# Performance work log

Measured on AMD Instinct MI355X. Metric: run time of the kernel, lower is better.

## Reference

```python
import jax, jax.numpy as jnp
import numpy as np

B, T, C = 2, 2048, 1024
NH = 16
HS = C // NH

def setup_inputs() -> dict:
    key = jax.random.key(0)
    ks = jax.random.split(key, 5)
    x = jax.random.normal(ks[0], (B, T, C), dtype=jnp.float32)
    scale = 1.0 / np.sqrt(C)
    Wk = jax.random.normal(ks[1], (C, C), dtype=jnp.float32) * scale
    bk = jax.random.normal(ks[2], (C,), dtype=jnp.float32) * scale
    Wv = jax.random.normal(ks[3], (C, C), dtype=jnp.float32) * scale
    bv = jax.random.normal(ks[4], (C,), dtype=jnp.float32) * scale
    return {"x": x, "Wk": Wk, "bk": bk, "Wv": Wv, "bv": bv}

def reference(x, Wk, bk, Wv, bv):
    b, t, c = x.shape
    # projections: key and value are Dense; query is identity (as in source)
    k = (x @ Wk + bk).reshape(b, t, NH, HS).transpose(0, 2, 1, 3)  # b nh T hs
    q = x.reshape(b, t, NH, HS).transpose(0, 2, 1, 3)              # b nh T hs
    v = (x @ Wv + bv).reshape(b, t, NH, HS).transpose(0, 2, 1, 3)  # b nh T hs
    # NOTE: source computes logits = K @ Q^T (no 1/sqrt(d) scaling)
    logits = jnp.einsum('bhid,bhjd->bhij', k, q)                   # b nh T T
    causal = jnp.tril(jnp.ones((t, t), dtype=bool))                # True where allowed
    masked = jnp.where(causal[None, None, :, :], logits, -jnp.inf)
    att = jax.nn.softmax(masked, axis=-1)
    y = jnp.einsum('bhij,bhjd->bhid', att, v)                      # b nh T hs
    return y.transpose(0, 2, 1, 3).reshape(b, t, c)
```

## Files before the change

### kernel.cpp

```cpp
#include <hip/hip_runtime.h>
#include <cstdint>
#include <cstddef>

#define BB  2
#define TT  2048
#define CC  1024
#define NHH 16
#define HSS 64
#define BT  (BB*TT)

typedef unsigned short u16;
typedef unsigned int u32;
typedef _Float16 f16;
typedef __attribute__((ext_vector_type(8))) _Float16 f16x8;
typedef __attribute__((ext_vector_type(8))) __bf16 bf16x8;
typedef __attribute__((ext_vector_type(4))) float f32x4;

__device__ __forceinline__ u16 f2bf(float f) {
    union { float f; u32 u; } x; x.f = f;
    return (u16)((x.u + 0x7fffu + ((x.u >> 16) & 1u)) >> 16);
}
__device__ __forceinline__ u16 f2h(float f) {
    union { f16 h; u16 u; } x; x.h = (f16)f;
    return x.u;
}
__device__ __forceinline__ u32 cvtpk_bf16(float lo, float hi) {
    u32 r;
    asm("v_cvt_pk_bf16_f32 %0, %1, %2" : "=v"(r) : "v"(lo), "v"(hi));
    return r;
}

#define MFMA_BF(a,b,c) __builtin_amdgcn_mfma_f32_16x16x32_bf16((a),(b),(c),0,0,0)
#define MFMA_F16(a,b,c) __builtin_amdgcn_mfma_f32_16x16x32_f16((a),(b),(c),0,0,0)

__device__ __forceinline__ void gld16(const u16* g, u16* l) {
    __builtin_amdgcn_global_load_lds(
        (const __attribute__((address_space(1))) unsigned int*)g,
        (__attribute__((address_space(3))) unsigned int*)l, 16, 0, 0);
}

__global__ __launch_bounds__(256) void convert_x(
    const float* __restrict__ X, u16* __restrict__ Xf)
{
    const int idx = (blockIdx.x * 256 + threadIdx.x) * 8;
    const float4 a = *(const float4*)&X[idx];
    const float4 b = *(const float4*)&X[idx + 4];
    float v[8] = {a.x, a.y, a.z, a.w, b.x, b.y, b.z, b.w};
    union { uint4 u; u16 s[8]; } H;
    #pragma unroll
    for (int u = 0; u < 8; ++u) H.s[u] = f2h(v[u]);
    *(uint4*)&Xf[idx] = H.u;
}

__global__ __launch_bounds__(256) void convert_w(
    const float* __restrict__ Wk, const float* __restrict__ Wv,
    u16* __restrict__ WkT, u16* __restrict__ WvT)
{
    const bool isK = (blockIdx.z == 0);
    const float* W = isK ? Wk : Wv;
    u16* WT = isK ? WkT : WvT;
    __shared__ __align__(16) u16 LH[64][72];
    const int tid = threadIdx.x;
    const int k0 = blockIdx.y * 64, n0 = blockIdx.x * 64;
    {
        const int row = tid >> 2, coff = (tid & 3) * 16;
        const float* g = &W[(size_t)(k0 + row) * CC + n0 + coff];
        #pragma unroll
        for (int u = 0; u < 16; ++u) LH[row][coff + u] = f2h(g[u]);
    }
    __syncthreads();
    {
        const int n = tid >> 2, kc = (tid & 3) * 16;
        union { uint4 u[2]; u16 s[16]; } Hq;
        #pragma unroll
        for (int u = 0; u < 16; ++u) Hq.s[u] = LH[kc + u][n];
        uint4* ph = (uint4*)&WT[(size_t)(n0 + n) * CC + k0 + kc];
        ph[0] = Hq.u[0]; ph[1] = Hq.u[1];
    }
}

__global__ __launch_bounds__(256) void proj_kernel(
    const u16* __restrict__ Xf, const u16* __restrict__ WkT,
    const u16* __restrict__ WvT,
    const float* __restrict__ bk, const float* __restrict__ bv,
    u16* __restrict__ Kf, u16* __restrict__ Vt)
{
    __shared__ u16 SM[4][8192];

    const int id = blockIdx.x;
    const int xcd = id & 7, idx = id >> 3;
    const int z = idx >> 5, rem = idx & 31;
    const int n0 = (rem & 7) * 128;
    const int m0 = (xcd * 4 + (rem >> 3)) * 128;
    const bool isK = (z == 0);
    const u16* WT = isK ? WkT : WvT;

    const int tid = threadIdx.x;
    const int w = tid >> 6, lane = tid & 63;
    const int quad = lane >> 4, l15 = lane & 15;
    const int wm = (w >> 1) * 64, wn = (w & 1) * 64;

    const u16* src = (w < 2) ? Xf : WT;
    const int rb = (w < 2) ? m0 : n0;
    int srow[8], scg[8];
    #pragma unroll
    for (int t = 0; t < 8; ++t) {
        int ci = (w & 1) * 512 + t * 64 + lane;
        srow[t] = ci >> 3;
        scg[t] = ((ci & 7) - srow[t]) & 7;
    }
    const int sbase = (w & 1) * 4096;

    f32x4 acc[4][4] = {};

    {
        u16* dst = ((w < 2) ? SM[0] : SM[2]) + sbase;
        #pragma unroll
        for (int t = 0; t < 8; ++t)
            gld16(src + (size_t)(rb + srow[t]) * CC + scg[t] * 8, dst + t * 512);
    }

    for (int ki = 0; ki < 16; ++ki) {
        const int buf = ki & 1;
        __syncthreads();
        if (ki < 15) {
            u16* dst = ((w < 2) ? SM[buf ^ 1] : SM[2 + (buf ^ 1)]) + sbase;
            const int k0n = (ki + 1) * 64;
            #pragma unroll
            for (int t = 0; t < 8; ++t)
                gld16(src + (size_t)(rb + srow[t]) * CC + k0n + scg[t] * 8,
                      dst + t * 512);
        }
        const u16* Ab = SM[buf];
        const u16* Bb = SM[2 + buf];
        #pragma unroll
        for (int kk = 0; kk < 2; ++kk) {
            f16x8 ah[4];
            #pragma unroll
            for (int i = 0; i < 4; ++i) {
                const int row = wm + i * 16 + l15;
                const int cp = ((kk * 4 + quad + row) & 7) * 8;
                ah[i] = *(const f16x8*)&Ab[row * 64 + cp];
            }
            #pragma unroll
            for (int j = 0; j < 4; ++j) {
                const int rowb = wn + j * 16 + l15;
                const int cpb = ((kk * 4 + quad + rowb) & 7) * 8;
                f16x8 bh_ = *(const f16x8*)&Bb[rowb * 64 + cpb];
                #pragma unroll
                for (int i = 0; i < 4; ++i)
                    acc[i][j] = MFMA_F16(ah[i], bh_, acc[i][j]);
            }
        }
    }

    __syncthreads();
    u16* XL = &SM[0][0];

    if (isK) {
        #pragma unroll
        for (int j = 0; j < 4; ++j) {
            const float bias = bk[n0 + wn + j * 16 + l15];
            #pragma unroll
            for (int i = 0; i < 4; ++i)
                #pragma unroll
                for (int r = 0; r < 4; ++r)
                    XL[(wm + i * 16 + quad * 4 + r) * 136 + wn + j * 16 + l15] =
                        f2h(acc[i][j][r] + bias);
        }
        __syncthreads();
        const int r = tid >> 1, half = tid & 1;
        #pragma unroll
        for (int t = 0; t < 8; ++t)
            *(uint4*)&Kf[(size_t)(m0 + r) * CC + n0 + half * 64 + t * 8] =
                *(const uint4*)&XL[r * 136 + half * 64 + t * 8];
    } else {
        #pragma unroll
        for (int j = 0; j < 4; ++j) {
            const float bias = bv[n0 + wn + j * 16 + l15];
            #pragma unroll
            for (int i = 0; i < 4; ++i) {
                uint2 pk;
                pk.x = (u32)f2bf(acc[i][j][0] + bias) |
                       ((u32)f2bf(acc[i][j][1] + bias) << 16);
                pk.y = (u32)f2bf(acc[i][j][2] + bias) |
                       ((u32)f2bf(acc[i][j][3] + bias) << 16);
                *(uint2*)&XL[(wn + j * 16 + l15) * 136 + wm + i * 16 + quad * 4] = pk;
            }
        }
        __syncthreads();
        const int nl = tid >> 1, half = tid & 1;
        const int d = (n0 + nl) & (HSS - 1), hh = (n0 + nl) >> 6;
        const int bb = m0 >> 11, tb = (m0 & (TT - 1)) + half * 64;
        const size_t gb = ((size_t)(bb * NHH + hh) * HSS + d) * TT + tb;
        #pragma unroll
        for (int t = 0; t < 8; ++t)
            *(uint4*)&Vt[gb + t * 8] = *(const uint4*)&XL[nl * 136 + half * 64 + t * 8];
    }
}

__global__ __launch_bounds__(256) void attn_kernel(
    const u16* __restrict__ Xf, const u16* __restrict__ Kf,
    const u16* __restrict__ Vt, float* __restrict__ out)
{
    __shared__ u16 Xs[2][4096];
    __shared__ u16 Vs[2][4096];
    __shared__ __align__(16) u16 Ps[4][2][1152];

    const int L = blockIdx.x;
    const int xcd = L & 7, k = (L >> 3) & 15, grp = L >> 7;
    const int hb = xcd + 8 * grp;
    const int h = hb & (NHH - 1), b = hb >> 4;
    const int iA = k, iB = 31 - k;
    const int i0A = iA * 64, i0B = iB * 64;

    const int tid = threadIdx.x;
    const int w = tid >> 6, lane = tid & 63;
    const int quad = lane >> 4, l15 = lane & 15;
    const size_t rowbase = (size_t)b * TT;
    const int hd = h * HSS;
    const size_t vgbase = (size_t)(b * NHH + h) * HSS * TT;

    bf16x8 ones;
    { union { u32 u[4]; bf16x8 v; } o;
      #pragma unroll
      for (int i = 0; i < 4; ++i) o.u[i] = 0x3F803F80u;
      ones = o.v; }

    f16x8 qA[2], qB[2];
    #pragma unroll
    for (int c = 0; c < 2; ++c) {
        qA[c] = *(const f16x8*)&Kf[(rowbase + i0A + w * 16 + l15) * CC + hd + c * 32 + quad * 8];
        qB[c] = *(const f16x8*)&Kf[(rowbase + i0B + w * 16 + l15) * CC + hd + c * 32 + quad * 8];
    }

    int crow[2], ccg[2], cbase[2];
    #pragma unroll
    for (int t = 0; t < 2; ++t) {
        const int ci = t * 256 + tid;
        crow[t] = ci >> 3;
        ccg[t] = ((ci & 7) - crow[t]) & 7;
        cbase[t] = (t * 256 + w * 64) * 8;
    }
    const u16* gx[2]; const u16* gv[2];
    #pragma unroll
    for (int t = 0; t < 2; ++t) {
        gx[t] = Xf + (rowbase + crow[t]) * CC + hd + ccg[t] * 8;
        gv[t] = Vt + vgbase + (size_t)crow[t] * TT + ccg[t] * 8;
    }

    #pragma unroll
    for (int t = 0; t < 2; ++t) {
        gld16(gx[t], Xs[0] + cbase[t]);
        gld16(gv[t], Vs[0] + cbase[t]);
    }

    f32x4 oA[4] = {}, oB[4] = {};
    f32x4 laA = {}, laB = {};

    for (int jt = 0; jt <= iB; ++jt) {
        const int buf = jt & 1;
        __syncthreads();
        if (jt < iB) {
            const int j0n = (jt + 1) * 64;
            #pragma unroll
            for (int t = 0; t < 2; ++t) {
                gld16(gx[t] + (size_t)j0n * CC, Xs[buf ^ 1] + cbase[t]);
                gld16(gv[t] + j0n, Vs[buf ^ 1] + cbase[t]);
            }
        }
        const bool doA = (jt <= iA);

        f32x4 sB[4], sA[4];
        #pragma unroll
        for (int nt = 0; nt < 4; ++nt) {
            const int krow = nt * 16 + l15;
            f16x8 x0 = *(const f16x8*)&Xs[buf][krow * 64 + ((quad + krow) & 7) * 8];
            f16x8 x1 = *(const f16x8*)&Xs[buf][krow * 64 + ((quad + 4 + krow) & 7) * 8];
            f32x4 z = {-20.f, -20.f, -20.f, -20.f};
            z = MFMA_F16(x0, qB[0], z);
            z = MFMA_F16(x1, qB[1], z);
            sB[nt] = z;
            if (doA) {
                f32x4 y = {-20.f, -20.f, -20.f, -20.f};
                y = MFMA_F16(x0, qA[0], y);
                y = MFMA_F16(x1, qA[1], y);
                sA[nt] = y;
            }
        }
        if (jt == iB) {
            #pragma unroll
            for (int nt = 0; nt < 4; ++nt)
                #pragma unroll
                for (int r = 0; r < 4; ++r)
                    if (nt * 16 + quad * 4 + r > w * 16 + l15) sB[nt][r] = -1e30f;
        }
        if (doA && jt == iA) {
            #pragma unroll
            for (int nt = 0; nt < 4; ++nt)
                #pragma unroll
                for (int r = 0; r < 4; ++r)
                    if (nt * 16 + quad * 4 + r > w * 16 + l15) sA[nt][r] = -1e30f;
        }

        #pragma unroll
        for (int nt = 0; nt < 4; ++nt) {
            const float p0 = __expf(sB[nt][0]);
            const float p1 = __expf(sB[nt][1]);
            const float p2 = __expf(sB[nt][2]);
            const float p3 = __expf(sB[nt][3]);
            uint2 pk;
            pk.x = cvtpk_bf16(p0, p1);
            pk.y = cvtpk_bf16(p2, p3);
            *(uint2*)&Ps[w][0][l15 * 72 + nt * 16 + quad * 4] = pk;
        }
        if (doA) {
            #pragma unroll
            for (int nt = 0; nt < 4; ++nt) {
                const float p0 = __expf(sA[nt][0]);
                const float p1 = __expf(sA[nt][1]);
                const float p2 = __expf(sA[nt][2]);
                const float p3 = __expf(sA[nt][3]);
                uint2 pk;
                pk.x = cvtpk_bf16(p0, p1);
                pk.y = cvtpk_bf16(p2, p3);
                *(uint2*)&Ps[w][1][l15 * 72 + nt * 16 + quad * 4] = pk;
            }
        }

        bf16x8 aB0 = *(const bf16x8*)&Ps[w][0][l15 * 72 + quad * 8];
        bf16x8 aB1 = *(const bf16x8*)&Ps[w][0][l15 * 72 + 32 + quad * 8];
        laB = MFMA_BF(aB0, ones, laB);
        laB = MFMA_BF(aB1, ones, laB);
        bf16x8 aA0, aA1;
        if (doA) {
            aA0 = *(const bf16x8*)&Ps[w][1][l15 * 72 + quad * 8];
            aA1 = *(const bf16x8*)&Ps[w][1][l15 * 72 + 32 + quad * 8];
            laA = MFMA_BF(aA0, ones, laA);
            laA = MFMA_BF(aA1, ones, laA);
        }

        #pragma unroll
        for (int dt = 0; dt < 4; ++dt) {
            const int vrow = dt * 16 + l15;
            bf16x8 v0 = *(const bf16x8*)&Vs[buf][vrow * 64 + ((quad + vrow) & 7) * 8];
            bf16x8 v1 = *(const bf16x8*)&Vs[buf][vrow * 64 + ((quad + 4 + vrow) & 7) * 8];
            oB[dt] = MFMA_BF(aB0, v0, oB[dt]);
            oB[dt] = MFMA_BF(aB1, v1, oB[dt]);
            if (doA) {
                oA[dt] = MFMA_BF(aA0, v0, oA[dt]);
                oA[dt] = MFMA_BF(aA1, v1, oA[dt]);
            }
        }
    }

    float liA[4], liB[4];
    #pragma unroll
    for (int r = 0; r < 4; ++r) { liA[r] = 1.f / laA[r]; liB[r] = 1.f / laB[r]; }
    #pragma unroll
    for (int dt = 0; dt < 4; ++dt) {
        #pragma unroll
        for (int r = 0; r < 4; ++r) {
            const int igA = i0A + w * 16 + quad * 4 + r;
            const int igB = i0B + w * 16 + quad * 4 + r;
            out[(rowbase + igA) * CC + hd + dt * 16 + l15] = oA[dt][r] * liA[r];
            out[(rowbase + igB) * CC + hd + dt * 16 + l15] = oB[dt][r] * liB[r];
        }
    }
}

extern "C" void kernel_launch(void* const* d_in, const int* in_sizes, int n_in,
                              void* d_out, int out_size, void* d_ws, size_t ws_size,
                              hipStream_t stream) {
    (void)in_sizes; (void)n_in; (void)out_size; (void)ws_size;
    const float* x  = (const float*)d_in[0];
    const float* Wk = (const float*)d_in[1];
    const float* bk = (const float*)d_in[2];
    const float* Wv = (const float*)d_in[3];
    const float* bv = (const float*)d_in[4];
    float* out = (float*)d_out;

    const size_t M4 = (size_t)BT * CC;
    const size_t M1 = (size_t)CC * CC;
    u16* Xf  = (u16*)d_ws;
    u16* Kf  = Xf + M4;
    u16* Vt  = Kf + M4;
    u16* WkT = Vt + M4;
    u16* WvT = WkT + M1;

    convert_x<<<dim3(M4 / (256 * 8)), 256, 0, stream>>>(x, Xf);
    convert_w<<<dim3(16, 16, 2), 256, 0, stream>>>(Wk, Wv, WkT, WvT);
    proj_kernel<<<dim3(512), 256, 0, stream>>>(Xf, WkT, WvT, bk, bv, Kf, Vt);
    attn_kernel<<<dim3(512), 256, 0, stream>>>(Xf, Kf, Vt, out);
}
```

Baseline: 150.1 us.

## Split attention key range across two blocks and combine partials

Each attention work item is split in two by interleaving key tiles (even/odd) across twice as many blocks. Each block writes unnormalized partial outputs and row sums to workspace, and a new combine kernel sums the two halves and normalizes. This is meant to raise parallelism and occupancy on the many-CU GPU. In exchange it adds an extra kernel launch plus writing and re-reading two fp32 partial output tensors. It relies on a fixed softmax offset rather than a running max, which is what makes the partial sums directly addable.

```diff
diff --git a/kernel.cpp b/kernel.cpp
--- a/kernel.cpp
+++ b/kernel.cpp
@@ -201,14 +201,16 @@
 
 __global__ __launch_bounds__(256) void attn_kernel(
     const u16* __restrict__ Xf, const u16* __restrict__ Kf,
-    const u16* __restrict__ Vt, float* __restrict__ out)
+    const u16* __restrict__ Vt, float* __restrict__ po,
+    float* __restrict__ pl)
 {
     __shared__ u16 Xs[2][4096];
     __shared__ u16 Vs[2][4096];
     __shared__ __align__(16) u16 Ps[4][2][1152];
 
     const int L = blockIdx.x;
-    const int xcd = L & 7, k = (L >> 3) & 15, grp = L >> 7;
+    const int xcd = L & 7, k = (L >> 3) & 15;
+    const int half = (L >> 7) & 1, grp = L >> 8;
     const int hb = xcd + 8 * grp;
     const int h = hb & (NHH - 1), b = hb >> 4;
     const int iA = k, iB = 31 - k;
@@ -249,20 +251,23 @@
         gv[t] = Vt + vgbase + (size_t)crow[t] * TT + ccg[t] * 8;
     }
 
-    #pragma unroll
-    for (int t = 0; t < 2; ++t) {
-        gld16(gx[t], Xs[0] + cbase[t]);
-        gld16(gv[t], Vs[0] + cbase[t]);
+    {
+        const int j0 = half * 64;
+        #pragma unroll
+        for (int t = 0; t < 2; ++t) {
+            gld16(gx[t] + (size_t)j0 * CC, Xs[0] + cbase[t]);
+            gld16(gv[t] + j0, Vs[0] + cbase[t]);
+        }
     }
 
     f32x4 oA[4] = {}, oB[4] = {};
     f32x4 laA = {}, laB = {};
 
-    for (int jt = 0; jt <= iB; ++jt) {
-        const int buf = jt & 1;
+    for (int jt = half; jt <= iB; jt += 2) {
+        const int buf = (jt >> 1) & 1;
         __syncthreads();
-        if (jt < iB) {
-            const int j0n = (jt + 1) * 64;
+        if (jt + 2 <= iB) {
+            const int j0n = (jt + 2) * 64;
             #pragma unroll
             for (int t = 0; t < 2; ++t) {
                 gld16(gx[t] + (size_t)j0n * CC, Xs[buf ^ 1] + cbase[t]);
@@ -354,19 +359,45 @@
         }
     }
 
-    float liA[4], liB[4];
-    #pragma unroll
-    for (int r = 0; r < 4; ++r) { liA[r] = 1.f / laA[r]; liB[r] = 1.f / laB[r]; }
     #pragma unroll
     for (int dt = 0; dt < 4; ++dt) {
         #pragma unroll
         for (int r = 0; r < 4; ++r) {
             const int igA = i0A + w * 16 + quad * 4 + r;
             const int igB = i0B + w * 16 + quad * 4 + r;
-            out[(rowbase + igA) * CC + hd + dt * 16 + l15] = oA[dt][r] * liA[r];
-            out[(rowbase + igB) * CC + hd + dt * 16 + l15] = oB[dt][r] * liB[r];
-        }
-    }
+            po[((size_t)half * BT + rowbase + igA) * CC + hd + dt * 16 + l15] = oA[dt][r];
+            po[((size_t)half * BT + rowbase + igB) * CC + hd + dt * 16 + l15] = oB[dt][r];
+        }
+    }
+    if (l15 == 0) {
+        #pragma unroll
+        for (int r = 0; r < 4; ++r) {
+            const int igA = i0A + w * 16 + quad * 4 + r;
+            const int igB = i0B + w * 16 + quad * 4 + r;
+            pl[((size_t)half * BT + rowbase + igA) * NHH + h] = laA[r];
+            pl[((size_t)half * BT + rowbase + igB) * NHH + h] = laB[r];
+        }
+    }
+}
+
+__global__ __launch_bounds__(256) void combine_kernel(
+    const float* __restrict__ po, const float* __restrict__ pl,
+    float* __restrict__ out)
+{
+    const int gid = blockIdx.x * 256 + threadIdx.x;
+    const int row = gid >> 8, c4 = gid & 255;
+    const int h = c4 >> 4;
+    const float l0 = pl[(size_t)row * NHH + h];
+    const float l1 = pl[(size_t)(BT + row) * NHH + h];
+    const float inv = 1.f / (l0 + l1);
+    const float4 o0 = *(const float4*)&po[(size_t)row * CC + c4 * 4];
+    const float4 o1 = *(const float4*)&po[(size_t)(BT + row) * CC + c4 * 4];
+    float4 o;
+    o.x = (o0.x + o1.x) * inv;
+    o.y = (o0.y + o1.y) * inv;
+    o.z = (o0.z + o1.z) * inv;
+    o.w = (o0.w + o1.w) * inv;
+    *(float4*)&out[(size_t)row * CC + c4 * 4] = o;
 }
 
 extern "C" void kernel_launch(void* const* d_in, const int* in_sizes, int n_in,
@@ -387,9 +418,12 @@
     u16* Vt  = Kf + M4;
     u16* WkT = Vt + M4;
     u16* WvT = WkT + M1;
+    float* po = (float*)(WvT + M1);
+    float* pl = po + (size_t)2 * BT * CC;
 
     convert_x<<<dim3(M4 / (256 * 8)), 256, 0, stream>>>(x, Xf);
     convert_w<<<dim3(16, 16, 2), 256, 0, stream>>>(Wk, Wv, WkT, WvT);
     proj_kernel<<<dim3(512), 256, 0, stream>>>(Xf, WkT, WvT, bk, bv, Kf, Vt);
-    attn_kernel<<<dim3(512), 256, 0, stream>>>(Xf, Kf, Vt, out);
-}
+    attn_kernel<<<dim3(1024), 256, 0, stream>>>(Xf, Kf, Vt, po, pl);
+    combine_kernel<<<dim3(4096), 256, 0, stream>>>(po, pl, out);
+}
```

New measurement: 157.3 us. 4.8% more time.
